# Optimization experiments

Measured on AMD Instinct MI355X. Metric: run time of the kernel, lower is better.

Reference implementation:

```python
import jax, jax.numpy as jnp
import numpy as np
from jax import lax

B, N, S = 4, 16384, 4096
D1, D2 = 128, 256
MLP = (256, 128)
EPS_W = 1e-8
EPS_BN = 1e-5
BIG = 1e8


def setup_inputs() -> dict:
    key = jax.random.key(0)
    ks = jax.random.split(key, 10)
    inp = {
        "xyz1": jax.random.normal(ks[0], (B, 3, N), jnp.float32),
        "xyz2": jax.random.normal(ks[1], (B, 3, S), jnp.float32),
        "points1": jax.random.normal(ks[2], (B, D1, N), jnp.float32),
        "points2": jax.random.normal(ks[3], (B, D2, S), jnp.float32),
        "idx1": jnp.repeat(jnp.arange(B, dtype=jnp.int32), N).reshape(B, N),
        "idx2": jnp.repeat(jnp.arange(B, dtype=jnp.int32), S).reshape(B, S),
    }
    cin = D1 + D2
    inp["w1"] = jax.random.normal(ks[4], (MLP[0], cin), jnp.float32) * 0.05
    inp["b1"] = jnp.zeros((MLP[0],), jnp.float32)
    inp["g1"] = jnp.ones((MLP[0],), jnp.float32)
    inp["be1"] = jnp.zeros((MLP[0],), jnp.float32)
    inp["w2"] = jax.random.normal(ks[5], (MLP[1], MLP[0]), jnp.float32) * 0.05
    inp["b2"] = jnp.zeros((MLP[1],), jnp.float32)
    inp["g2"] = jnp.ones((MLP[1],), jnp.float32)
    inp["be2"] = jnp.zeros((MLP[1],), jnp.float32)
    return inp


def _bn_relu(x, gamma, beta):
    # training-mode batchnorm over (B, N) per channel, then relu; x: [B, C, N]
    mean = jnp.mean(x, axis=(0, 2), keepdims=True)
    var = jnp.var(x, axis=(0, 2), keepdims=True)  # biased, as torch BN
    xn = (x - mean) * lax.rsqrt(var + EPS_BN)
    return jax.nn.relu(xn * gamma[None, :, None] + beta[None, :, None])


def _fp_forward(xyz1, xyz2, points1, points2, idx1, idx2,
                w1, b1, g1, be1, w2, b2, g2, be2):
    x1 = jnp.transpose(xyz1, (0, 2, 1))  # [B, N, 3]
    x2 = jnp.transpose(xyz2, (0, 2, 1))  # [B, S, 3]
    p2 = jnp.transpose(points2, (0, 2, 1))  # [B, S, D2]

    # squared pairwise distances [B, N, S]
    d = -2.0 * jnp.einsum('bnc,bsc->bns', x1, x2)
    d = d + jnp.sum(x1 * x1, -1)[:, :, None] + jnp.sum(x2 * x2, -1)[:, None, :]
    d = jnp.where(idx1[:, :, None] == idx2[:, None, :], d, jnp.inf)

    # 3 nearest neighbors (top-k on negated distances == sort-ascending take 3)
    neg_d3, idx3 = lax.top_k(-d, 3)          # [B, N, 3]
    d3 = -neg_d3
    recip = 1.0 / (d3 + EPS_W)
    weight = recip / jnp.sum(recip, axis=2, keepdims=True)
    weight = jnp.where(d3 > BIG, 0.0, weight)
    weight = jnp.nan_to_num(weight)

    gathered = jax.vmap(lambda p, i: p[i])(p2, idx3)   # [B, N, 3, D2]
    interp = jnp.sum(gathered * weight[..., None], axis=2)  # [B, N, D2]

    newp = jnp.concatenate([jnp.transpose(points1, (0, 2, 1)), interp], axis=-1)
    newp = jnp.transpose(newp, (0, 2, 1))  # [B, D1+D2, N]

    # 1x1 conv -> BN -> relu, twice
    h = jnp.einsum('bcn,oc->bon', newp, w1) + b1[None, :, None]
    h = _bn_relu(h, g1, be1)
    h = jnp.einsum('bcn,oc->bon', h, w2) + b2[None, :, None]
    h = _bn_relu(h, g2, be2)
    return h


def reference(xyz1, xyz2, points1, points2, idx1, idx2,
              w1, b1, g1, be1, w2, b2, g2, be2):
    return _fp_forward(xyz1, xyz2, points1, points2, idx1, idx2,
                       w1, b1, g1, be1, w2, b2, g2, be2)
```

## Files before the change

### kernel.cpp

```cpp
#include <hip/hip_runtime.h>
#include <hip/hip_bf16.h>

#define INF_F (__builtin_inff())

typedef __attribute__((ext_vector_type(8))) short bf16x8;
typedef __attribute__((ext_vector_type(4))) float f32x4;

__device__ __forceinline__ unsigned short f2bf(float f) {
  __hip_bfloat16 h = __float2bfloat16(f);
  return __builtin_bit_cast(unsigned short, h);
}
__device__ __forceinline__ float bf2f(unsigned short u) {
  return __uint_as_float((unsigned)u << 16);
}

#define TOP3_INS(d, sj, E0, E1, E2, J0, J1, J2)                      \
  {                                                                  \
    bool l0 = (d) < E0, l1 = (d) < E1;                               \
    E2 = l1 ? E1 : (d); J2 = l1 ? J1 : (sj);                         \
    E1 = l0 ? E0 : (l1 ? (d) : E1); J1 = l0 ? J0 : (l1 ? (sj) : J1); \
    E0 = l0 ? (d) : E0; J0 = l0 ? (sj) : J0;                         \
  }


__global__ __launch_bounds__(256) void transpose_k(const float* __restrict__ in,
                                                   unsigned short* __restrict__ out) {
  __shared__ float tile[32][33];
  int b = blockIdx.z;
  int s0 = blockIdx.x * 32;
  int k0 = blockIdx.y * 32;
  int tx = threadIdx.x, ty = threadIdx.y;
  const float* src = in + ((size_t)b * 256 + k0) * 4096 + s0;
  for (int r = ty; r < 32; r += 8) tile[r][tx] = src[(size_t)r * 4096 + tx];
  __syncthreads();
  unsigned short* dst = out + ((size_t)b * 4096 + s0) * 256 + k0;
  for (int r = ty; r < 32; r += 8) dst[(size_t)r * 256 + tx] = f2bf(tile[tx][r]);
}

__global__ __launch_bounds__(256) void p1t_k(const float* __restrict__ p1,
                                             unsigned short* __restrict__ X) {
  __shared__ float tile[32][33];
  int b = blockIdx.z;
  int n0 = blockIdx.x * 32;
  int c0 = blockIdx.y * 32;
  int tx = threadIdx.x, ty = threadIdx.y;
  const float* src = p1 + ((size_t)b * 128 + c0) * 16384 + n0;
  for (int r = ty; r < 32; r += 8) tile[r][tx] = src[(size_t)r * 16384 + tx];
  __syncthreads();
  for (int r = ty; r < 32; r += 8)
    X[((size_t)(b * 16384 + n0 + r)) * 384 + c0 + tx] = f2bf(tile[tx][r]);
}

__global__ __launch_bounds__(256) void wcvtpack_k(const float* __restrict__ w1,
                                                  const float* __restrict__ w2,
                                                  const float* __restrict__ xyz2,
                                                  const int* __restrict__ idx1,
                                                  const int* __restrict__ idx2,
                                                  unsigned short* __restrict__ w1b,
                                                  unsigned short* __restrict__ w2b,
                                                  float4* __restrict__ pack) {
  int id = blockIdx.x * 256 + threadIdx.x;
  if (id < 98304) {
    w1b[id] = f2bf(w1[id]);
  } else if (id < 131072) {
    w2b[id - 98304] = f2bf(w2[id - 98304]);
  } else {
    int pid = id - 131072;
    int b = pid >> 12, s = pid & 4095;
    float x = xyz2[(b * 3 + 0) * 4096 + s];
    float y = xyz2[(b * 3 + 1) * 4096 + s];
    float z = xyz2[(b * 3 + 2) * 4096 + s];
    float w = fmaf(x, x, fmaf(y, y, z * z));
    int common = idx1[b * 16384];
    w = (idx2[b * 4096 + s] == common) ? w : 3e38f;
    pack[b * 4096 + s] = make_float4(x, y, z, w);
  }
}

__global__ __launch_bounds__(256) void knn_k(const float* __restrict__ xyz1,
                                             const float* __restrict__ xyz2,
                                             const int* __restrict__ idx1,
                                             const int* __restrict__ idx2,
                                             const float4* __restrict__ pack,
                                             float* __restrict__ rec) {
  int bid = blockIdx.x;
  int qg = bid >> 3, sl = bid & 7;
  int b = qg >> 6;
  int nloc = (qg & 63) << 8;
  int t = threadIdx.x;
  int n = nloc + t;
  int q0i = b * 16384 + n;
  int common = idx1[b * 16384];
  int sbase = sl << 9;
  const float4* ps = pack + b * 4096 + sbase;
  float px = xyz1[(b * 3 + 0) * 16384 + n];
  float py = xyz1[(b * 3 + 1) * 16384 + n];
  float pz = xyz1[(b * 3 + 2) * 16384 + n];
  int myid = idx1[q0i];
  float pn = fmaf(px, px, fmaf(py, py, pz * pz));
  float qx = -2.f * px, qy = -2.f * py, qz = -2.f * pz;
  float e0 = INF_F, e1 = INF_F, e2 = INF_F;
  int j0 = 0, j1 = 0, j2 = 0;
#pragma unroll 8
  for (int s = 0; s < 512; ++s) {
    float4 p = ps[s];
    float d = fmaf(qx, p.x, fmaf(qy, p.y, fmaf(qz, p.z, pn))) + p.w;
    if (__builtin_expect(d < e2, 0)) {
      int sj = sbase + s;
      TOP3_INS(d, sj, e0, e1, e2, j0, j1, j2);
    }
  }
  if (__builtin_expect(myid != common, 0)) {
    e0 = INF_F; e1 = INF_F; e2 = INF_F; j0 = 0; j1 = 0; j2 = 0;
    for (int s = 0; s < 512; ++s) {
      int gs = sbase + s;
      float x = xyz2[(b * 3 + 0) * 4096 + gs];
      float y = xyz2[(b * 3 + 1) * 4096 + gs];
      float z = xyz2[(b * 3 + 2) * 4096 + gs];
      float w = fmaf(x, x, fmaf(y, y, z * z));
      float d = fmaf(qx, x, fmaf(qy, y, fmaf(qz, z, pn))) + w;
      d = (idx2[b * 4096 + gs] == myid) ? d : INF_F;
      if (d < e2) TOP3_INS(d, gs, e0, e1, e2, j0, j1, j2);
    }
  }
  float* r = &rec[((size_t)sl * 65536 + q0i) * 6];
  r[0] = e0; r[1] = e1; r[2] = e2;
  ((int*)r)[3] = j0; ((int*)r)[4] = j1; ((int*)r)[5] = j2;
}

__global__ __launch_bounds__(256) void knnmerge_k(const float* __restrict__ rec,
                                                  int* __restrict__ idx3,
                                                  float* __restrict__ wgt) {
  int i = blockIdx.x * 256 + threadIdx.x;
  float e0, e1, e2;
  int j0, j1, j2;
  {
    const float* r = &rec[(size_t)i * 6];
    e0 = r[0]; e1 = r[1]; e2 = r[2];
    j0 = ((const int*)r)[3]; j1 = ((const int*)r)[4]; j2 = ((const int*)r)[5];
  }
#pragma unroll
  for (int c = 1; c < 8; ++c) {
    const float* r = &rec[((size_t)c * 65536 + i) * 6];
    const int* ir = (const int*)r;
#pragma unroll
    for (int w = 0; w < 3; ++w) {
      float d = r[w];
      int sj = ir[3 + w];
      bool l0 = (d < e0) || (d == e0 && sj < j0);
      bool l1 = (d < e1) || (d == e1 && sj < j1);
      bool l2 = (d < e2) || (d == e2 && sj < j2);
      e2 = l1 ? e1 : (l2 ? d : e2);
      j2 = l1 ? j1 : (l2 ? sj : j2);
      e1 = l0 ? e0 : (l1 ? d : e1);
      j1 = l0 ? j0 : (l1 ? sj : j1);
      e0 = l0 ? d : e0;
      j0 = l0 ? sj : j0;
    }
  }
  float r0 = 1.f / (e0 + 1e-8f);
  float r1 = 1.f / (e1 + 1e-8f);
  float r2 = 1.f / (e2 + 1e-8f);
  float rs = r0 + r1 + r2;
  float w0 = (e0 > 1e8f) ? 0.f : r0 / rs;
  float w1 = (e1 > 1e8f) ? 0.f : r1 / rs;
  float w2 = (e2 > 1e8f) ? 0.f : r2 / rs;
  idx3[(size_t)i * 3 + 0] = j0; idx3[(size_t)i * 3 + 1] = j1; idx3[(size_t)i * 3 + 2] = j2;
  wgt[(size_t)i * 3 + 0] = w0;  wgt[(size_t)i * 3 + 1] = w1;  wgt[(size_t)i * 3 + 2] = w2;
}

__global__ __launch_bounds__(256) void interp_k(const unsigned short* __restrict__ p2t,
                                                const int* __restrict__ idx3,
                                                const float* __restrict__ wgt,
                                                unsigned short* __restrict__ X) {
  int i0 = blockIdx.x * 128;
  int b = i0 >> 14;
  int k = threadIdx.x;
  const unsigned short* base = p2t + (size_t)b * 4096 * 256;
#pragma unroll 2
  for (int ii = 0; ii < 128; ++ii) {
    int i = i0 + ii;
    int id0 = idx3[i * 3 + 0], id1 = idx3[i * 3 + 1], id2 = idx3[i * 3 + 2];
    float w0 = wgt[i * 3 + 0], w1v = wgt[i * 3 + 1], w2v = wgt[i * 3 + 2];
    float v = w0 * bf2f(base[id0 * 256 + k]);
    v = fmaf(w1v, bf2f(base[id1 * 256 + k]), v);
    v = fmaf(w2v, bf2f(base[id2 * 256 + k]), v);
    X[(size_t)i * 384 + 128 + k] = f2bf(v);
  }
}

__global__ __launch_bounds__(256) void gemm1_k(const unsigned short* __restrict__ X,
                                               const unsigned short* __restrict__ Wb,
                                               unsigned short* __restrict__ h1T) {
  __shared__ unsigned short sW[128][40];
  __shared__ unsigned short sX[128][40];
  int t = threadIdx.x;
  int i0 = blockIdx.x * 128;
  int c0 = blockIdx.y * 128;
  int w = t >> 6, lane = t & 63;
  int wc = (w & 1) * 64, wn = (w >> 1) * 64;
  int l15 = lane & 15, g = lane >> 4;
  f32x4 acc[4][4];
#pragma unroll
  for (int a = 0; a < 4; ++a)
#pragma unroll
    for (int bq = 0; bq < 4; ++bq) acc[a][bq] = (f32x4)0.f;
  int sr = t & 127, sh = t >> 7;
  for (int kc = 0; kc < 12; ++kc) {
    int k0 = kc * 32;
    __syncthreads();
    {
      const uint4* gw = (const uint4*)&Wb[(size_t)(c0 + sr) * 384 + k0 + sh * 16];
      uint4 v0 = gw[0], v1 = gw[1];
      *(uint4*)&sW[sr][sh * 16] = v0;
      *(uint4*)&sW[sr][sh * 16 + 8] = v1;
      const uint4* gx = (const uint4*)&X[(size_t)(i0 + sr) * 384 + k0 + sh * 16];
      uint4 x0 = gx[0], x1 = gx[1];
      *(uint4*)&sX[sr][sh * 16] = x0;
      *(uint4*)&sX[sr][sh * 16 + 8] = x1;
    }
    __syncthreads();
    bf16x8 a[4], b[4];
#pragma unroll
    for (int tm = 0; tm < 4; ++tm)
      a[tm] = *(const bf16x8*)&sW[wc + tm * 16 + l15][g * 8];
#pragma unroll
    for (int tn = 0; tn < 4; ++tn)
      b[tn] = *(const bf16x8*)&sX[wn + tn * 16 + l15][g * 8];
#pragma unroll
    for (int tm = 0; tm < 4; ++tm)
#pragma unroll
      for (int tn = 0; tn < 4; ++tn)
        acc[tm][tn] = __builtin_amdgcn_mfma_f32_16x16x32_bf16(a[tm], b[tn], acc[tm][tn], 0, 0, 0);
  }
#pragma unroll
  for (int tm = 0; tm < 4; ++tm)
#pragma unroll
    for (int tn = 0; tn < 4; ++tn) {
      int c = c0 + wc + tm * 16 + g * 4;
      int n = i0 + wn + tn * 16 + l15;
      f32x4 v = acc[tm][tn];
      ushort4 o;
      o.x = f2bf(v[0]); o.y = f2bf(v[1]); o.z = f2bf(v[2]); o.w = f2bf(v[3]);
      *(ushort4*)&h1T[(size_t)n * 256 + c] = o;
    }
}

__global__ __launch_bounds__(256) void bnstats1_k(const unsigned short* __restrict__ h,
                                                  float* __restrict__ part) {
  int t = threadIdx.x, q = t & 63, ro = t >> 6;
  int r0 = blockIdx.x * 256;
  float s0 = 0, s1 = 0, s2 = 0, s3 = 0, q0 = 0, q1 = 0, q2 = 0, q3 = 0;
  for (int it = 0; it < 64; ++it) {
    size_t r = r0 + it * 4 + ro;
    ushort4 v = *(const ushort4*)&h[r * 256 + q * 4];
    float f0 = bf2f(v.x), f1 = bf2f(v.y), f2 = bf2f(v.z), f3 = bf2f(v.w);
    s0 += f0; q0 += f0 * f0;
    s1 += f1; q1 += f1 * f1;
    s2 += f2; q2 += f2 * f2;
    s3 += f3; q3 += f3 * f3;
  }
  __shared__ float sm[256][8];
  sm[t][0] = s0; sm[t][1] = s1; sm[t][2] = s2; sm[t][3] = s3;
  sm[t][4] = q0; sm[t][5] = q1; sm[t][6] = q2; sm[t][7] = q3;
  __syncthreads();
  if (t < 64) {
#pragma unroll
    for (int j = 1; j < 4; ++j)
#pragma unroll
      for (int e = 0; e < 8; ++e) sm[t][e] += sm[t + 64 * j][e];
#pragma unroll
    for (int i = 0; i < 4; ++i) {
      part[((size_t)blockIdx.x * 256 + t * 4 + i) * 2 + 0] = sm[t][i];
      part[((size_t)blockIdx.x * 256 + t * 4 + i) * 2 + 1] = sm[t][4 + i];
    }
  }
}

__global__ __launch_bounds__(256) void bnstats2_k(const float* __restrict__ o2,
                                                  float* __restrict__ part) {
  int t = threadIdx.x, q = t & 31, ro = t >> 5;
  int r0 = blockIdx.x * 256;
  float s0 = 0, s1 = 0, s2 = 0, s3 = 0, q0 = 0, q1 = 0, q2 = 0, q3 = 0;
  for (int it = 0; it < 32; ++it) {
    size_t r = r0 + it * 8 + ro;
    float4 v = *(const float4*)&o2[r * 128 + q * 4];
    s0 += v.x; q0 += v.x * v.x;
    s1 += v.y; q1 += v.y * v.y;
    s2 += v.z; q2 += v.z * v.z;
    s3 += v.w; q3 += v.w * v.w;
  }
  __shared__ float sm[256][8];
  sm[t][0] = s0; sm[t][1] = s1; sm[t][2] = s2; sm[t][3] = s3;
  sm[t][4] = q0; sm[t][5] = q1; sm[t][6] = q2; sm[t][7] = q3;
  __syncthreads();
  if (t < 32) {
#pragma unroll
    for (int j = 1; j < 8; ++j)
#pragma unroll
      for (int e = 0; e < 8; ++e) sm[t][e] += sm[t + 32 * j][e];
#pragma unroll
    for (int i = 0; i < 4; ++i) {
      part[((size_t)blockIdx.x * 128 + t * 4 + i) * 2 + 0] = sm[t][i];
      part[((size_t)blockIdx.x * 128 + t * 4 + i) * 2 + 1] = sm[t][4 + i];
    }
  }
}

template <int C>
__global__ __launch_bounds__(256) void bnfold_k(const float* __restrict__ part,
                                                const float* __restrict__ g,
                                                const float* __restrict__ be,
                                                float* __restrict__ A,
                                                float* __restrict__ Cc) {
  int c = threadIdx.x;
  if (c >= C) return;
  float s1 = 0.f, s2 = 0.f;
  for (int b = 0; b < 256; ++b) {
    s1 += part[((size_t)b * C + c) * 2 + 0];
    s2 += part[((size_t)b * C + c) * 2 + 1];
  }
  float mean = s1 * (1.f / 65536.f);
  float var = s2 * (1.f / 65536.f) - mean * mean;
  float a = g[c] * rsqrtf(var + 1e-5f);
  A[c] = a;
  Cc[c] = be[c] - mean * a;
}

__global__ __launch_bounds__(256) void gemm2_k(const unsigned short* __restrict__ h1T,
                                               const unsigned short* __restrict__ Wb,
                                               const float* __restrict__ A,
                                               const float* __restrict__ C,
                                               float* __restrict__ o2) {
  __shared__ unsigned short sW[128][40];
  __shared__ unsigned short sX[128][40];
  int t = threadIdx.x;
  int i0 = blockIdx.x * 128;
  int w = t >> 6, lane = t & 63;
  int wc = (w & 1) * 64, wn = (w >> 1) * 64;
  int l15 = lane & 15, g = lane >> 4;
  f32x4 acc[4][4];
#pragma unroll
  for (int a = 0; a < 4; ++a)
#pragma unroll
    for (int bq = 0; bq < 4; ++bq) acc[a][bq] = (f32x4)0.f;
  int sr = t & 127, sh = t >> 7;
  for (int kc = 0; kc < 8; ++kc) {
    int k0 = kc * 32;
    int kcol = k0 + sh * 16;
    __syncthreads();
    {
      const uint4* gw = (const uint4*)&Wb[(size_t)sr * 256 + kcol];
      uint4 v0 = gw[0], v1 = gw[1];
      *(uint4*)&sW[sr][sh * 16] = v0;
      *(uint4*)&sW[sr][sh * 16 + 8] = v1;
      const uint4* gx = (const uint4*)&h1T[(size_t)(i0 + sr) * 256 + kcol];
      uint4 x0 = gx[0], x1 = gx[1];
      unsigned rr[8] = {x0.x, x0.y, x0.z, x0.w, x1.x, x1.y, x1.z, x1.w};
      unsigned ww[8];
#pragma unroll
      for (int e = 0; e < 8; ++e) {
        int ch = kcol + 2 * e;
        float f0 = bf2f((unsigned short)(rr[e] & 0xFFFFu));
        float f1 = bf2f((unsigned short)(rr[e] >> 16));
        f0 = fmaxf(fmaf(A[ch], f0, C[ch]), 0.f);
        f1 = fmaxf(fmaf(A[ch + 1], f1, C[ch + 1]), 0.f);
        ww[e] = (unsigned)f2bf(f0) | ((unsigned)f2bf(f1) << 16);
      }
      uint4 y0 = {ww[0], ww[1], ww[2], ww[3]};
      uint4 y1 = {ww[4], ww[5], ww[6], ww[7]};
      *(uint4*)&sX[sr][sh * 16] = y0;
      *(uint4*)&sX[sr][sh * 16 + 8] = y1;
    }
    __syncthreads();
    bf16x8 a[4], b[4];
#pragma unroll
    for (int tm = 0; tm < 4; ++tm)
      a[tm] = *(const bf16x8*)&sW[wc + tm * 16 + l15][g * 8];
#pragma unroll
    for (int tn = 0; tn < 4; ++tn)
      b[tn] = *(const bf16x8*)&sX[wn + tn * 16 + l15][g * 8];
#pragma unroll
    for (int tm = 0; tm < 4; ++tm)
#pragma unroll
      for (int tn = 0; tn < 4; ++tn)
        acc[tm][tn] = __builtin_amdgcn_mfma_f32_16x16x32_bf16(a[tm], b[tn], acc[tm][tn], 0, 0, 0);
  }
#pragma unroll
  for (int tm = 0; tm < 4; ++tm)
#pragma unroll
    for (int tn = 0; tn < 4; ++tn) {
      int c = wc + tm * 16 + g * 4;
      int n = i0 + wn + tn * 16 + l15;
      f32x4 v = acc[tm][tn];
      *(float4*)&o2[(size_t)n * 128 + c] = make_float4(v[0], v[1], v[2], v[3]);
    }
}

__global__ __launch_bounds__(256) void final_k(const float* __restrict__ o2,
                                               const float* __restrict__ A,
                                               const float* __restrict__ C,
                                               float* __restrict__ out) {
  __shared__ float tile[32][33];
  int b = blockIdx.z;
  int n0 = blockIdx.x * 32;
  int c0 = blockIdx.y * 32;
  int tx = threadIdx.x, ty = threadIdx.y;
  float a = A[c0 + tx], cc = C[c0 + tx];
  for (int r = ty; r < 32; r += 8) {
    float v = o2[(size_t)(b * 16384 + n0 + r) * 128 + c0 + tx];
    tile[r][tx] = fmaxf(fmaf(a, v, cc), 0.f);
  }
  __syncthreads();
  for (int r = ty; r < 32; r += 8)
    out[((size_t)(b * 128 + c0 + r)) * 16384 + n0 + tx] = tile[tx][r];
}

extern "C" void kernel_launch(void* const* d_in, const int* in_sizes, int n_in,
                              void* d_out, int out_size, void* d_ws, size_t ws_size,
                              hipStream_t stream) {
  const float* xyz1 = (const float*)d_in[0];
  const float* xyz2 = (const float*)d_in[1];
  const float* p1   = (const float*)d_in[2];
  const float* p2   = (const float*)d_in[3];
  const int*   idx1 = (const int*)d_in[4];
  const int*   idx2 = (const int*)d_in[5];
  const float* w1   = (const float*)d_in[6];
  const float* g1   = (const float*)d_in[8];
  const float* be1  = (const float*)d_in[9];
  const float* w2   = (const float*)d_in[10];
  const float* g2   = (const float*)d_in[12];
  const float* be2  = (const float*)d_in[13];
  float* out = (float*)d_out;

  char* ws = (char*)d_ws;
  int*            idx3 = (int*)(ws + 0x0);
  float*          wgt  = (float*)(ws + 0xC0000);
  unsigned short* X    = (unsigned short*)(ws + 0x180000);
  unsigned short* h1T  = (unsigned short*)(ws + 0x3180000);
  unsigned short* p2t  = (unsigned short*)(ws + 0x3180000);
  float*          o2   = (float*)(ws + 0x5180000);
  float*          rec  = (float*)(ws + 0x5180000);
  unsigned short* w1b  = (unsigned short*)(ws + 0x7180000);
  unsigned short* w2b  = (unsigned short*)(ws + 0x71B0000);
  float*          part1 = (float*)(ws + 0x71C0000);
  float*          part2 = (float*)(ws + 0x7240000);
  float4*         pack = (float4*)(ws + 0x7280000);
  float*          a1   = (float*)(ws + 0x72C8000);
  float*          c1   = a1 + 256;
  float*          a2   = c1 + 256;
  float*          c2   = a2 + 128;

  hipLaunchKernelGGL(transpose_k, dim3(128, 8, 4), dim3(32, 8), 0, stream, p2, p2t);
  hipLaunchKernelGGL(wcvtpack_k, dim3(576), dim3(256), 0, stream,
                     w1, w2, xyz2, idx1, idx2, w1b, w2b, pack);
  hipLaunchKernelGGL(p1t_k, dim3(512, 4, 4), dim3(32, 8), 0, stream, p1, X);
  hipLaunchKernelGGL(knn_k, dim3(2048), dim3(256), 0, stream,
                     xyz1, xyz2, idx1, idx2, pack, rec);
  hipLaunchKernelGGL(knnmerge_k, dim3(256), dim3(256), 0, stream, rec, idx3, wgt);
  hipLaunchKernelGGL(interp_k, dim3(512), dim3(256), 0, stream, p2t, idx3, wgt, X);
  hipLaunchKernelGGL(gemm1_k, dim3(512, 2), dim3(256), 0, stream, X, w1b, h1T);
  hipLaunchKernelGGL(bnstats1_k, dim3(256), dim3(256), 0, stream, h1T, part1);
  hipLaunchKernelGGL((bnfold_k<256>), dim3(1), dim3(256), 0, stream, part1, g1, be1, a1, c1);
  hipLaunchKernelGGL(gemm2_k, dim3(512), dim3(256), 0, stream, h1T, w2b, a1, c1, o2);
  hipLaunchKernelGGL(bnstats2_k, dim3(256), dim3(256), 0, stream, o2, part2);
  hipLaunchKernelGGL((bnfold_k<128>), dim3(1), dim3(256), 0, stream, part2, g2, be2, a2, c2);
  hipLaunchKernelGGL(final_k, dim3(512, 4, 4), dim3(32, 8), 0, stream, o2, a2, c2, out);
}
```

Before: 260.4 us.

## Fuse prep kernels, merge knn-merge into interp, fold BN stats into GEMMs

```diff
diff --git a/kernel.cpp b/kernel.cpp
--- a/kernel.cpp
+++ b/kernel.cpp
@@ -23,57 +23,60 @@
   }
 
 
-__global__ __launch_bounds__(256) void transpose_k(const float* __restrict__ in,
-                                                   unsigned short* __restrict__ out) {
-  __shared__ float tile[32][33];
-  int b = blockIdx.z;
-  int s0 = blockIdx.x * 32;
-  int k0 = blockIdx.y * 32;
-  int tx = threadIdx.x, ty = threadIdx.y;
-  const float* src = in + ((size_t)b * 256 + k0) * 4096 + s0;
-  for (int r = ty; r < 32; r += 8) tile[r][tx] = src[(size_t)r * 4096 + tx];
-  __syncthreads();
-  unsigned short* dst = out + ((size_t)b * 4096 + s0) * 256 + k0;
-  for (int r = ty; r < 32; r += 8) dst[(size_t)r * 256 + tx] = f2bf(tile[tx][r]);
-}
-
-__global__ __launch_bounds__(256) void p1t_k(const float* __restrict__ p1,
-                                             unsigned short* __restrict__ X) {
-  __shared__ float tile[32][33];
-  int b = blockIdx.z;
-  int n0 = blockIdx.x * 32;
-  int c0 = blockIdx.y * 32;
-  int tx = threadIdx.x, ty = threadIdx.y;
-  const float* src = p1 + ((size_t)b * 128 + c0) * 16384 + n0;
-  for (int r = ty; r < 32; r += 8) tile[r][tx] = src[(size_t)r * 16384 + tx];
-  __syncthreads();
-  for (int r = ty; r < 32; r += 8)
-    X[((size_t)(b * 16384 + n0 + r)) * 384 + c0 + tx] = f2bf(tile[tx][r]);
-}
-
-__global__ __launch_bounds__(256) void wcvtpack_k(const float* __restrict__ w1,
-                                                  const float* __restrict__ w2,
-                                                  const float* __restrict__ xyz2,
-                                                  const int* __restrict__ idx1,
-                                                  const int* __restrict__ idx2,
-                                                  unsigned short* __restrict__ w1b,
-                                                  unsigned short* __restrict__ w2b,
-                                                  float4* __restrict__ pack) {
-  int id = blockIdx.x * 256 + threadIdx.x;
-  if (id < 98304) {
-    w1b[id] = f2bf(w1[id]);
-  } else if (id < 131072) {
-    w2b[id - 98304] = f2bf(w2[id - 98304]);
+__global__ __launch_bounds__(256) void prep_k(const float* __restrict__ p2,
+                                              const float* __restrict__ p1,
+                                              const float* __restrict__ w1,
+                                              const float* __restrict__ w2,
+                                              const float* __restrict__ xyz2,
+                                              const int* __restrict__ idx1,
+                                              const int* __restrict__ idx2,
+                                              unsigned short* __restrict__ p2t,
+                                              unsigned short* __restrict__ X,
+                                              unsigned short* __restrict__ w1b,
+                                              unsigned short* __restrict__ w2b,
+                                              float4* __restrict__ pack) {
+  int id = blockIdx.x;
+  int t = threadIdx.x;
+  if (id < 4096) {
+    __shared__ float tile[32][33];
+    int s0 = (id & 127) * 32;
+    int k0 = ((id >> 7) & 7) * 32;
+    int b = id >> 10;
+    int tx = t & 31, ty = t >> 5;
+    const float* src = p2 + ((size_t)b * 256 + k0) * 4096 + s0;
+    for (int r = ty; r < 32; r += 8) tile[r][tx] = src[(size_t)r * 4096 + tx];
+    __syncthreads();
+    unsigned short* dst = p2t + ((size_t)b * 4096 + s0) * 256 + k0;
+    for (int r = ty; r < 32; r += 8) dst[(size_t)r * 256 + tx] = f2bf(tile[tx][r]);
+  } else if (id < 12288) {
+    __shared__ float tile[32][33];
+    int id2 = id - 4096;
+    int n0 = (id2 & 511) * 32;
+    int c0 = ((id2 >> 9) & 3) * 32;
+    int b = id2 >> 11;
+    int tx = t & 31, ty = t >> 5;
+    const float* src = p1 + ((size_t)b * 128 + c0) * 16384 + n0;
+    for (int r = ty; r < 32; r += 8) tile[r][tx] = src[(size_t)r * 16384 + tx];
+    __syncthreads();
+    for (int r = ty; r < 32; r += 8)
+      X[((size_t)(b * 16384 + n0 + r)) * 384 + c0 + tx] = f2bf(tile[tx][r]);
   } else {
-    int pid = id - 131072;
-    int b = pid >> 12, s = pid & 4095;
-    float x = xyz2[(b * 3 + 0) * 4096 + s];
-    float y = xyz2[(b * 3 + 1) * 4096 + s];
-    float z = xyz2[(b * 3 + 2) * 4096 + s];
-    float w = fmaf(x, x, fmaf(y, y, z * z));
-    int common = idx1[b * 16384];
-    w = (idx2[b * 4096 + s] == common) ? w : 3e38f;
-    pack[b * 4096 + s] = make_float4(x, y, z, w);
+    int id3 = (id - 12288) * 256 + t;
+    if (id3 < 98304) {
+      w1b[id3] = f2bf(w1[id3]);
+    } else if (id3 < 131072) {
+      w2b[id3 - 98304] = f2bf(w2[id3 - 98304]);
+    } else {
+      int pid = id3 - 131072;
+      int b = pid >> 12, s = pid & 4095;
+      float x = xyz2[(b * 3 + 0) * 4096 + s];
+      float y = xyz2[(b * 3 + 1) * 4096 + s];
+      float z = xyz2[(b * 3 + 2) * 4096 + s];
+      float w = fmaf(x, x, fmaf(y, y, z * z));
+      int common = idx1[b * 16384];
+      w = (idx2[b * 4096 + s] == common) ? w : 3e38f;
+      pack[b * 4096 + s] = make_float4(x, y, z, w);
+    }
   }
 }
 
@@ -128,77 +131,77 @@
   ((int*)r)[3] = j0; ((int*)r)[4] = j1; ((int*)r)[5] = j2;
 }
 
-__global__ __launch_bounds__(256) void knnmerge_k(const float* __restrict__ rec,
-                                                  int* __restrict__ idx3,
-                                                  float* __restrict__ wgt) {
-  int i = blockIdx.x * 256 + threadIdx.x;
-  float e0, e1, e2;
-  int j0, j1, j2;
-  {
-    const float* r = &rec[(size_t)i * 6];
-    e0 = r[0]; e1 = r[1]; e2 = r[2];
-    j0 = ((const int*)r)[3]; j1 = ((const int*)r)[4]; j2 = ((const int*)r)[5];
-  }
-#pragma unroll
-  for (int c = 1; c < 8; ++c) {
-    const float* r = &rec[((size_t)c * 65536 + i) * 6];
-    const int* ir = (const int*)r;
-#pragma unroll
-    for (int w = 0; w < 3; ++w) {
-      float d = r[w];
-      int sj = ir[3 + w];
-      bool l0 = (d < e0) || (d == e0 && sj < j0);
-      bool l1 = (d < e1) || (d == e1 && sj < j1);
-      bool l2 = (d < e2) || (d == e2 && sj < j2);
-      e2 = l1 ? e1 : (l2 ? d : e2);
-      j2 = l1 ? j1 : (l2 ? sj : j2);
-      e1 = l0 ? e0 : (l1 ? d : e1);
-      j1 = l0 ? j0 : (l1 ? sj : j1);
-      e0 = l0 ? d : e0;
-      j0 = l0 ? sj : j0;
-    }
-  }
-  float r0 = 1.f / (e0 + 1e-8f);
-  float r1 = 1.f / (e1 + 1e-8f);
-  float r2 = 1.f / (e2 + 1e-8f);
-  float rs = r0 + r1 + r2;
-  float w0 = (e0 > 1e8f) ? 0.f : r0 / rs;
-  float w1 = (e1 > 1e8f) ? 0.f : r1 / rs;
-  float w2 = (e2 > 1e8f) ? 0.f : r2 / rs;
-  idx3[(size_t)i * 3 + 0] = j0; idx3[(size_t)i * 3 + 1] = j1; idx3[(size_t)i * 3 + 2] = j2;
-  wgt[(size_t)i * 3 + 0] = w0;  wgt[(size_t)i * 3 + 1] = w1;  wgt[(size_t)i * 3 + 2] = w2;
-}
-
-__global__ __launch_bounds__(256) void interp_k(const unsigned short* __restrict__ p2t,
-                                                const int* __restrict__ idx3,
-                                                const float* __restrict__ wgt,
-                                                unsigned short* __restrict__ X) {
+__global__ __launch_bounds__(256) void interpm_k(const float* __restrict__ rec,
+                                                 const unsigned short* __restrict__ p2t,
+                                                 unsigned short* __restrict__ X) {
+  __shared__ int sId[128][3];
+  __shared__ float sWt[128][3];
   int i0 = blockIdx.x * 128;
   int b = i0 >> 14;
-  int k = threadIdx.x;
+  int t = threadIdx.x;
+  if (t < 128) {
+    int i = i0 + t;
+    float e0, e1, e2;
+    int j0, j1, j2;
+    {
+      const float* r = &rec[(size_t)i * 6];
+      e0 = r[0]; e1 = r[1]; e2 = r[2];
+      j0 = ((const int*)r)[3]; j1 = ((const int*)r)[4]; j2 = ((const int*)r)[5];
+    }
+#pragma unroll
+    for (int c = 1; c < 8; ++c) {
+      const float* r = &rec[((size_t)c * 65536 + i) * 6];
+      const int* ir = (const int*)r;
+#pragma unroll
+      for (int w = 0; w < 3; ++w) {
+        float d = r[w];
+        int sj = ir[3 + w];
+        bool l0 = (d < e0) || (d == e0 && sj < j0);
+        bool l1 = (d < e1) || (d == e1 && sj < j1);
+        bool l2 = (d < e2) || (d == e2 && sj < j2);
+        e2 = l1 ? e1 : (l2 ? d : e2);
+        j2 = l1 ? j1 : (l2 ? sj : j2);
+        e1 = l0 ? e0 : (l1 ? d : e1);
+        j1 = l0 ? j0 : (l1 ? sj : j1);
+        e0 = l0 ? d : e0;
+        j0 = l0 ? sj : j0;
+      }
+    }
+    float r0 = 1.f / (e0 + 1e-8f);
+    float r1 = 1.f / (e1 + 1e-8f);
+    float r2 = 1.f / (e2 + 1e-8f);
+    float rs = r0 + r1 + r2;
+    sWt[t][0] = (e0 > 1e8f) ? 0.f : r0 / rs;
+    sWt[t][1] = (e1 > 1e8f) ? 0.f : r1 / rs;
+    sWt[t][2] = (e2 > 1e8f) ? 0.f : r2 / rs;
+    sId[t][0] = j0; sId[t][1] = j1; sId[t][2] = j2;
+  }
+  __syncthreads();
+  int k = t;
   const unsigned short* base = p2t + (size_t)b * 4096 * 256;
 #pragma unroll 2
   for (int ii = 0; ii < 128; ++ii) {
-    int i = i0 + ii;
-    int id0 = idx3[i * 3 + 0], id1 = idx3[i * 3 + 1], id2 = idx3[i * 3 + 2];
-    float w0 = wgt[i * 3 + 0], w1v = wgt[i * 3 + 1], w2v = wgt[i * 3 + 2];
+    int id0 = sId[ii][0], id1 = sId[ii][1], id2 = sId[ii][2];
+    float w0 = sWt[ii][0], w1v = sWt[ii][1], w2v = sWt[ii][2];
     float v = w0 * bf2f(base[id0 * 256 + k]);
     v = fmaf(w1v, bf2f(base[id1 * 256 + k]), v);
     v = fmaf(w2v, bf2f(base[id2 * 256 + k]), v);
-    X[(size_t)i * 384 + 128 + k] = f2bf(v);
+    X[(size_t)(i0 + ii) * 384 + 128 + k] = f2bf(v);
   }
 }
 
 __global__ __launch_bounds__(256) void gemm1_k(const unsigned short* __restrict__ X,
                                                const unsigned short* __restrict__ Wb,
-                                               unsigned short* __restrict__ h1T) {
+                                               unsigned short* __restrict__ h1T,
+                                               float* __restrict__ part1) {
   __shared__ unsigned short sW[128][40];
   __shared__ unsigned short sX[128][40];
   int t = threadIdx.x;
   int i0 = blockIdx.x * 128;
   int c0 = blockIdx.y * 128;
   int w = t >> 6, lane = t & 63;
-  int wc = (w & 1) * 64, wn = (w >> 1) * 64;
+  int wc = (w & 1) * 64, wni = w >> 1;
+  int wn = wni * 64;
   int l15 = lane & 15, g = lane >> 4;
   f32x4 acc[4][4];
 #pragma unroll
@@ -244,70 +247,49 @@
       o.x = f2bf(v[0]); o.y = f2bf(v[1]); o.z = f2bf(v[2]); o.w = f2bf(v[3]);
       *(ushort4*)&h1T[(size_t)n * 256 + c] = o;
     }
-}
-
-__global__ __launch_bounds__(256) void bnstats1_k(const unsigned short* __restrict__ h,
-                                                  float* __restrict__ part) {
-  int t = threadIdx.x, q = t & 63, ro = t >> 6;
-  int r0 = blockIdx.x * 256;
-  float s0 = 0, s1 = 0, s2 = 0, s3 = 0, q0 = 0, q1 = 0, q2 = 0, q3 = 0;
-  for (int it = 0; it < 64; ++it) {
-    size_t r = r0 + it * 4 + ro;
-    ushort4 v = *(const ushort4*)&h[r * 256 + q * 4];
-    float f0 = bf2f(v.x), f1 = bf2f(v.y), f2 = bf2f(v.z), f3 = bf2f(v.w);
-    s0 += f0; q0 += f0 * f0;
-    s1 += f1; q1 += f1 * f1;
-    s2 += f2; q2 += f2 * f2;
-    s3 += f3; q3 += f3 * f3;
-  }
-  __shared__ float sm[256][8];
-  sm[t][0] = s0; sm[t][1] = s1; sm[t][2] = s2; sm[t][3] = s3;
-  sm[t][4] = q0; sm[t][5] = q1; sm[t][6] = q2; sm[t][7] = q3;
-  __syncthreads();
-  if (t < 64) {
-#pragma unroll
-    for (int j = 1; j < 4; ++j)
-#pragma unroll
-      for (int e = 0; e < 8; ++e) sm[t][e] += sm[t + 64 * j][e];
-#pragma unroll
-    for (int i = 0; i < 4; ++i) {
-      part[((size_t)blockIdx.x * 256 + t * 4 + i) * 2 + 0] = sm[t][i];
-      part[((size_t)blockIdx.x * 256 + t * 4 + i) * 2 + 1] = sm[t][4 + i];
-    }
-  }
-}
-
-__global__ __launch_bounds__(256) void bnstats2_k(const float* __restrict__ o2,
-                                                  float* __restrict__ part) {
-  int t = threadIdx.x, q = t & 31, ro = t >> 5;
-  int r0 = blockIdx.x * 256;
-  float s0 = 0, s1 = 0, s2 = 0, s3 = 0, q0 = 0, q1 = 0, q2 = 0, q3 = 0;
-  for (int it = 0; it < 32; ++it) {
-    size_t r = r0 + it * 8 + ro;
-    float4 v = *(const float4*)&o2[r * 128 + q * 4];
-    s0 += v.x; q0 += v.x * v.x;
-    s1 += v.y; q1 += v.y * v.y;
-    s2 += v.z; q2 += v.z * v.z;
-    s3 += v.w; q3 += v.w * v.w;
-  }
-  __shared__ float sm[256][8];
-  sm[t][0] = s0; sm[t][1] = s1; sm[t][2] = s2; sm[t][3] = s3;
-  sm[t][4] = q0; sm[t][5] = q1; sm[t][6] = q2; sm[t][7] = q3;
-  __syncthreads();
-  if (t < 32) {
-#pragma unroll
-    for (int j = 1; j < 8; ++j)
-#pragma unroll
-      for (int e = 0; e < 8; ++e) sm[t][e] += sm[t + 32 * j][e];
-#pragma unroll
-    for (int i = 0; i < 4; ++i) {
-      part[((size_t)blockIdx.x * 128 + t * 4 + i) * 2 + 0] = sm[t][i];
-      part[((size_t)blockIdx.x * 128 + t * 4 + i) * 2 + 1] = sm[t][4 + i];
-    }
-  }
-}
-
-template <int C>
+  float s_[4][4], q_[4][4];
+#pragma unroll
+  for (int tm = 0; tm < 4; ++tm)
+#pragma unroll
+    for (int j = 0; j < 4; ++j) {
+      float s = 0.f, q = 0.f;
+#pragma unroll
+      for (int tn = 0; tn < 4; ++tn) {
+        float v = acc[tm][tn][j];
+        s += v; q = fmaf(v, v, q);
+      }
+      s_[tm][j] = s; q_[tm][j] = q;
+    }
+#pragma unroll
+  for (int mask = 1; mask < 16; mask <<= 1)
+#pragma unroll
+    for (int tm = 0; tm < 4; ++tm)
+#pragma unroll
+      for (int j = 0; j < 4; ++j) {
+        s_[tm][j] += __shfl_xor(s_[tm][j], mask);
+        q_[tm][j] += __shfl_xor(q_[tm][j], mask);
+      }
+  __syncthreads();
+  float* red = (float*)&sW[0][0];
+  if (l15 == 0) {
+#pragma unroll
+    for (int tm = 0; tm < 4; ++tm)
+#pragma unroll
+      for (int j = 0; j < 4; ++j) {
+        int cl = wc + tm * 16 + g * 4 + j;
+        red[(wni * 128 + cl) * 2 + 0] = s_[tm][j];
+        red[(wni * 128 + cl) * 2 + 1] = q_[tm][j];
+      }
+  }
+  __syncthreads();
+  if (t < 256) {
+    int cl = t >> 1, st = t & 1;
+    float v = red[(0 * 128 + cl) * 2 + st] + red[(1 * 128 + cl) * 2 + st];
+    part1[((size_t)blockIdx.x * 256 + c0 + cl) * 2 + st] = v;
+  }
+}
+
+template <int C, int NB>
 __global__ __launch_bounds__(256) void bnfold_k(const float* __restrict__ part,
                                                 const float* __restrict__ g,
                                                 const float* __restrict__ be,
@@ -316,7 +298,7 @@
   int c = threadIdx.x;
   if (c >= C) return;
   float s1 = 0.f, s2 = 0.f;
-  for (int b = 0; b < 256; ++b) {
+  for (int b = 0; b < NB; ++b) {
     s1 += part[((size_t)b * C + c) * 2 + 0];
     s2 += part[((size_t)b * C + c) * 2 + 1];
   }
@@ -331,13 +313,15 @@
                                                const unsigned short* __restrict__ Wb,
                                                const float* __restrict__ A,
                                                const float* __restrict__ C,
-                                               float* __restrict__ o2) {
+                                               float* __restrict__ o2,
+                                               float* __restrict__ part2) {
   __shared__ unsigned short sW[128][40];
   __shared__ unsigned short sX[128][40];
   int t = threadIdx.x;
   int i0 = blockIdx.x * 128;
   int w = t >> 6, lane = t & 63;
-  int wc = (w & 1) * 64, wn = (w >> 1) * 64;
+  int wc = (w & 1) * 64, wni = w >> 1;
+  int wn = wni * 64;
   int l15 = lane & 15, g = lane >> 4;
   f32x4 acc[4][4];
 #pragma unroll
@@ -395,6 +379,46 @@
       f32x4 v = acc[tm][tn];
       *(float4*)&o2[(size_t)n * 128 + c] = make_float4(v[0], v[1], v[2], v[3]);
     }
+  float s_[4][4], q_[4][4];
+#pragma unroll
+  for (int tm = 0; tm < 4; ++tm)
+#pragma unroll
+    for (int j = 0; j < 4; ++j) {
+      float s = 0.f, q = 0.f;
+#pragma unroll
+      for (int tn = 0; tn < 4; ++tn) {
+        float v = acc[tm][tn][j];
+        s += v; q = fmaf(v, v, q);
+      }
+      s_[tm][j] = s; q_[tm][j] = q;
+    }
+#pragma unroll
+  for (int mask = 1; mask < 16; mask <<= 1)
+#pragma unroll
+    for (int tm = 0; tm < 4; ++tm)
+#pragma unroll
+      for (int j = 0; j < 4; ++j) {
+        s_[tm][j] += __shfl_xor(s_[tm][j], mask);
+        q_[tm][j] += __shfl_xor(q_[tm][j], mask);
+      }
+  __syncthreads();
+  float* red = (float*)&sW[0][0];
+  if (l15 == 0) {
+#pragma unroll
+    for (int tm = 0; tm < 4; ++tm)
+#pragma unroll
+      for (int j = 0; j < 4; ++j) {
+        int cl = wc + tm * 16 + g * 4 + j;
+        red[(wni * 128 + cl) * 2 + 0] = s_[tm][j];
+        red[(wni * 128 + cl) * 2 + 1] = q_[tm][j];
+      }
+  }
+  __syncthreads();
+  if (t < 256) {
+    int cl = t >> 1, st = t & 1;
+    float v = red[(0 * 128 + cl) * 2 + st] + red[(1 * 128 + cl) * 2 + st];
+    part2[((size_t)blockIdx.x * 128 + cl) * 2 + st] = v;
+  }
 }
 
 __global__ __launch_bounds__(256) void final_k(const float* __restrict__ o2,
@@ -434,8 +458,6 @@
   float* out = (float*)d_out;
 
   char* ws = (char*)d_ws;
-  int*            idx3 = (int*)(ws + 0x0);
-  float*          wgt  = (float*)(ws + 0xC0000);
   unsigned short* X    = (unsigned short*)(ws + 0x180000);
   unsigned short* h1T  = (unsigned short*)(ws + 0x3180000);
   unsigned short* p2t  = (unsigned short*)(ws + 0x3180000);
@@ -444,26 +466,24 @@
   unsigned short* w1b  = (unsigned short*)(ws + 0x7180000);
   unsigned short* w2b  = (unsigned short*)(ws + 0x71B0000);
   float*          part1 = (float*)(ws + 0x71C0000);
-  float*          part2 = (float*)(ws + 0x7240000);
-  float4*         pack = (float4*)(ws + 0x7280000);
-  float*          a1   = (float*)(ws + 0x72C8000);
+  float*          part2 = (float*)(ws + 0x72C0000);
+  float4*         pack = (float4*)(ws + 0x7340000);
+  float*          a1   = (float*)(ws + 0x7388000);
   float*          c1   = a1 + 256;
   float*          a2   = c1 + 256;
   float*          c2   = a2 + 128;
 
-  hipLaunchKernelGGL(transpose_k, dim3(128, 8, 4), dim3(32, 8), 0, stream, p2, p2t);
-  hipLaunchKernelGGL(wcvtpack_k, dim3(576), dim3(256), 0, stream,
-                     w1, w2, xyz2, idx1, idx2, w1b, w2b, pack);
-  hipLaunchKernelGGL(p1t_k, dim3(512, 4, 4), dim3(32, 8), 0, stream, p1, X);
+  hipLaunchKernelGGL(prep_k, dim3(12864), dim3(256), 0, stream,
+                     p2, p1, w1, w2, xyz2, idx1, idx2, p2t, X, w1b, w2b, pack);
   hipLaunchKernelGGL(knn_k, dim3(2048), dim3(256), 0, stream,
                      xyz1, xyz2, idx1, idx2, pack, rec);
-  hipLaunchKernelGGL(knnmerge_k, dim3(256), dim3(256), 0, stream, rec, idx3, wgt);
-  hipLaunchKernelGGL(interp_k, dim3(512), dim3(256), 0, stream, p2t, idx3, wgt, X);
-  hipLaunchKernelGGL(gemm1_k, dim3(512, 2), dim3(256), 0, stream, X, w1b, h1T);
-  hipLaunchKernelGGL(bnstats1_k, dim3(256), dim3(256), 0, stream, h1T, part1);
-  hipLaunchKernelGGL((bnfold_k<256>), dim3(1), dim3(256), 0, stream, part1, g1, be1, a1, c1);
-  hipLaunchKernelGGL(gemm2_k, dim3(512), dim3(256), 0, stream, h1T, w2b, a1, c1, o2);
-  hipLaunchKernelGGL(bnstats2_k, dim3(256), dim3(256), 0, stream, o2, part2);
-  hipLaunchKernelGGL((bnfold_k<128>), dim3(1), dim3(256), 0, stream, part2, g2, be2, a2, c2);
+  hipLaunchKernelGGL(interpm_k, dim3(512), dim3(256), 0, stream, rec, p2t, X);
+  hipLaunchKernelGGL(gemm1_k, dim3(512, 2), dim3(256), 0, stream, X, w1b, h1T, part1);
+  hipLaunchKernelGGL((bnfold_k<256, 512>), dim3(1), dim3(256), 0, stream,
+                     part1, g1, be1, a1, c1);
+  hipLaunchKernelGGL(gemm2_k, dim3(512), dim3(256), 0, stream,
+                     h1T, w2b, a1, c1, o2, part2);
+  hipLaunchKernelGGL((bnfold_k<128, 512>), dim3(1), dim3(256), 0, stream,
+                     part2, g2, be2, a2, c2);
   hipLaunchKernelGGL(final_k, dim3(512, 4, 4), dim3(32, 8), 0, stream, o2, a2, c2, out);
 }
```

After: 249.6 us. 4.1% less time.
